# Kernel optimization log

Measured on AMD Instinct MI355X. Metric: run time of the kernel, lower is better.

## Reference

```python
import jax, jax.numpy as jnp
import numpy as np


def setup_inputs() -> dict:
    key = jax.random.key(0)
    ks = jax.random.split(key, 5)
    B, C, H, W = 4, 64, 64, 64
    C8 = C // 8
    return {
        "x_opt": jax.random.normal(ks[0], (B, C, H, W), jnp.float32),
        "x_sar": jax.random.normal(ks[1], (B, C, H, W), jnp.float32),
        "wq": jax.random.normal(ks[2], (C8, C), jnp.float32) * 0.05,
        "bq": jnp.zeros((C8,), jnp.float32),
        "wk": jax.random.normal(ks[3], (C8, C), jnp.float32) * 0.05,
        "bk": jnp.zeros((C8,), jnp.float32),
        "wv": jax.random.normal(ks[4], (C, C), jnp.float32) * 0.05,
        "bv": jnp.zeros((C,), jnp.float32),
        "gamma": jnp.zeros((1,), jnp.float32),
    }


def reference(x_opt, x_sar, wq, bq, wk, bk, wv, bv, gamma):
    b, c, h, w = x_opt.shape
    n = h * w
    xo = x_opt.reshape(b, c, n)  # [b, c, N]
    xs = x_sar.reshape(b, c, n)
    # 1x1 convs == channel matmuls
    q = jnp.einsum('oc,bcn->bon', wq, xo) + bq[None, :, None]  # [b, c//8, N]
    k = jnp.einsum('oc,bcn->bon', wk, xs) + bk[None, :, None]  # [b, c//8, N]
    v = jnp.einsum('oc,bcn->bon', wv, xs) + bv[None, :, None]  # [b, c, N]
    # attn[b, n, m] = softmax_m( q[:, :, n] . k[:, :, m] )  -- NO 1/sqrt(d) scaling
    scores = jnp.einsum('bdn,bdm->bnm', q, k)  # [b, N, N]
    attn = jax.nn.softmax(scores, axis=-1)
    # out[b, c, n] = sum_m v[b, c, m] * attn[b, n, m]
    out = jnp.einsum('bcm,bnm->bcn', v, attn).reshape(b, c, h, w)
    return gamma[0] * out + x_opt
```

## Files before the change

### kernel.cpp

```cpp
#include <hip/hip_runtime.h>
#include <hip/hip_bf16.h>
#include <stdint.h>

#define NDIM 4096
#define CDIM 64
#define NSPLIT 8
#define SPAN (NDIM / NSPLIT)
#define KBLK 128
#define NIT (SPAN / KBLK)
#define LOG2E 1.44269504088896f

typedef float f32x16 __attribute__((ext_vector_type(16)));
typedef short bf16x8 __attribute__((ext_vector_type(8)));
union U4B { uint4 u; bf16x8 b; };

static __device__ __forceinline__ uint32_t cvtpk(float lo, float hi) {
  uint32_t r;
  asm("v_cvt_pk_bf16_f32 %0, %1, %2" : "=v"(r) : "v"(lo), "v"(hi));
  return r;
}
static __device__ __forceinline__ uint16_t f2bf(float f) {
  uint32_t r;
  asm("v_cvt_pk_bf16_f32 %0, %1, %1" : "=v"(r) : "v"(f));
  return (uint16_t)r;
}
static __device__ __forceinline__ float fexp2(float x) {
  return __builtin_amdgcn_exp2f(x);
}
static __device__ __forceinline__ void gload_lds16(const void* g, void* l) {
  __builtin_amdgcn_global_load_lds(
      (const __attribute__((address_space(1))) uint32_t*)g,
      (__attribute__((address_space(3))) uint32_t*)l, 16, 0, 0);
}

__global__ __launch_bounds__(256) void proj_kernel(
    const float* __restrict__ x_opt, const float* __restrict__ x_sar,
    const float* __restrict__ wq, const float* __restrict__ bq,
    const float* __restrict__ wk, const float* __restrict__ bk,
    const float* __restrict__ wvp, const float* __restrict__ bv,
    uint16_t* __restrict__ qf, uint16_t* __restrict__ kf,
    uint16_t* __restrict__ vf)
{
  const int tid = threadIdx.x;
  const int w = tid >> 6;
  const int l = tid & 63;
  const int x = l & 31;
  const int hi = l >> 5;

  const int id = blockIdx.x;
  const int b = id >> 7;
  const int n0 = (id & 127) * 32;
  const size_t xbase = (size_t)b * CDIM * NDIM;

  const float* xsrc = (w == 2) ? x_opt : x_sar;
  bf16x8 xB[4];
#pragma unroll
  for (int kc = 0; kc < 4; kc++) {
    float sv[8];
#pragma unroll
    for (int j = 0; j < 8; j++)
      sv[j] = xsrc[xbase + (size_t)(kc * 16 + hi * 8 + j) * NDIM + n0 + x];
    U4B us;
    us.u = make_uint4(cvtpk(sv[0], sv[1]), cvtpk(sv[2], sv[3]),
                      cvtpk(sv[4], sv[5]), cvtpk(sv[6], sv[7]));
    xB[kc] = us.b;
  }

  bf16x8 aF[4];
#pragma unroll
  for (int kc = 0; kc < 4; kc++) {
    U4B ua;
    ua.u = make_uint4(0u, 0u, 0u, 0u);
    if (w < 2) {
      const float* wr = wvp + (w * 32 + x) * 64 + kc * 16 + hi * 8;
      float4 wa = ((const float4*)wr)[0];
      float4 wb = ((const float4*)wr)[1];
      ua.u = make_uint4(cvtpk(wa.x, wa.y), cvtpk(wa.z, wa.w),
                        cvtpk(wb.x, wb.y), cvtpk(wb.z, wb.w));
    } else if (x < 8) {
      const float* wr = ((w == 2) ? wq : wk) + x * 64 + kc * 16 + hi * 8;
      float4 wa = ((const float4*)wr)[0];
      float4 wb = ((const float4*)wr)[1];
      ua.u = make_uint4(cvtpk(wa.x, wa.y), cvtpk(wa.z, wa.w),
                        cvtpk(wb.x, wb.y), cvtpk(wb.z, wb.w));
    }
    aF[kc] = ua.b;
  }

  const f32x16 z16 = {0.f,0.f,0.f,0.f, 0.f,0.f,0.f,0.f,
                      0.f,0.f,0.f,0.f, 0.f,0.f,0.f,0.f};
  f32x16 acc = z16;
#pragma unroll
  for (int kc = 0; kc < 4; kc++)
    acc = __builtin_amdgcn_mfma_f32_32x32x16_bf16(aF[kc], xB[kc], acc, 0, 0, 0);

  if (w < 2) {
#pragma unroll
    for (int r = 0; r < 16; r++) {
      const int row = w * 32 + (r & 3) + 8 * (r >> 2) + 4 * hi;
      vf[(size_t)(b * 64 + row) * NDIM + n0 + x] = f2bf(acc[r] + bv[row]);
    }
  } else {
    const float* bias = (w == 2) ? bq : bk;
    const float scl = (w == 2) ? LOG2E : 1.0f;
    float gv[4];
#pragma unroll
    for (int r = 0; r < 4; r++) gv[r] = (acc[r] + bias[4 * hi + r]) * scl;
    uint16_t* dst = (w == 2) ? qf : kf;
    const size_t nrow = ((size_t)b * NDIM + n0 + x) * 16;
    uint2 st;
    st.x = cvtpk(gv[0], gv[1]); st.y = cvtpk(gv[2], gv[3]);
    *(uint2*)(dst + nrow + hi * 4) = st;
    if (hi == 0) {
      const uint4 z4 = make_uint4(0u, 0u, 0u, 0u);
      *(uint4*)(dst + nrow + 8) = z4;
    }
  }
}

__global__ __launch_bounds__(256, 4) void attn_kernel(
    const uint16_t* __restrict__ qf, const uint16_t* __restrict__ kf,
    const uint16_t* __restrict__ vf,
    uint16_t* __restrict__ po, float* __restrict__ ls)
{
  __shared__ __align__(16) uint16_t vt[2][64][128];

  const int tid = threadIdx.x;
  const int w = tid >> 6;
  const int l = tid & 63;
  const int x = l & 31;
  const int hi = l >> 5;

  const int id = blockIdx.x;
  const int sp = id & 7;
  const int qb = (id >> 3) & 31;
  const int b = id >> 8;

  const int n0 = qb * 128;
  const uint16_t* vsrc = vf + (size_t)b * CDIM * NDIM + sp * SPAN;
  const uint16_t* ksrc = kf + ((size_t)b * NDIM + sp * SPAN) * 16;
  const int qrow = n0 + w * 32 + x;

  U4B qfr;
  qfr.u = *(const uint4*)(qf + ((size_t)b * NDIM + qrow) * 16 + hi * 8);

  const uint32_t xh4 = (uint32_t)(((x & 15) ^ hi) << 4);
  const uint8_t* vbase0 = (const uint8_t*)&vt[0][0][0] + (size_t)x * 256;
  const uint8_t* vbase1 = vbase0 + 16384;

  const f32x16 z16 = {0.f,0.f,0.f,0.f, 0.f,0.f,0.f,0.f,
                      0.f,0.f,0.f,0.f, 0.f,0.f,0.f,0.f};
  f32x16 oacc0 = z16, oacc1 = z16;
  float lacc[4] = {0.f, 0.f, 0.f, 0.f};

  auto stageV = [&](int t, int buf) {
#pragma unroll
    for (int si = 0; si < 4; si++) {
      const int rowbase = w * 16 + si * 4;
      const int row = rowbase + (l >> 4);
      gload_lds16(vsrc + (size_t)row * NDIM + t * KBLK +
                      (((l & 15) ^ (row & 15)) << 3),
                  &vt[buf][rowbase][0]);
    }
  };

  stageV(0, 0);
  uint4 kc = *(const uint4*)(ksrc + (size_t)x * 16 + hi * 8);
  __syncthreads();

#pragma unroll
  for (int gq = 0; gq < 16; gq++) {
    const int it = gq >> 2;
    const int q4 = gq & 3;

    if (q4 == 0 && it + 1 < NIT) stageV(it + 1, (it + 1) & 1);

    uint4 kn = *(const uint4*)(ksrc + ((size_t)(gq + 1) * 32 + x) * 16 + hi * 8);

    U4B ka; ka.u = kc;
    f32x16 s = __builtin_amdgcn_mfma_f32_32x32x16_bf16(ka.b, qfr.b, z16, 0, 0, 0);

    float p[16];
#pragma unroll
    for (int i = 0; i < 16; i++) p[i] = fexp2(s[i]);
    float t8[8];
#pragma unroll
    for (int i = 0; i < 8; i++) t8[i] = p[i] + p[i + 8];
#pragma unroll
    for (int i = 0; i < 4; i++) lacc[i] += t8[i] + t8[i + 4];

    uint32_t W[8];
#pragma unroll
    for (int j = 0; j < 8; j++) W[j] = cvtpk(p[2 * j], p[2 * j + 1]);

    const uint8_t* vb = (it & 1) ? vbase1 : vbase0;
    __builtin_amdgcn_s_setprio(1);
#pragma unroll
    for (int sub = 0; sub < 2; sub++) {
      uint32_t a0 = W[sub * 4 + 0], b0 = W[sub * 4 + 2];
      uint32_t a1 = W[sub * 4 + 1], b1 = W[sub * 4 + 3];
      asm("v_permlane32_swap_b32 %0, %1" : "+v"(a0), "+v"(b0));
      asm("v_permlane32_swap_b32 %0, %1" : "+v"(a1), "+v"(b1));
      U4B pf;
      pf.u = make_uint4(a0, a1, b0, b1);
      const uint32_t kb4 = (uint32_t)((q4 * 4 + sub * 2) << 4);
      const uint8_t* va = vb + (kb4 ^ xh4);
      U4B vf0, vf1;
      vf0.u = *(const uint4*)(va);
      vf1.u = *(const uint4*)(va + 8192);
      oacc0 = __builtin_amdgcn_mfma_f32_32x32x16_bf16(vf0.b, pf.b, oacc0, 0, 0, 0);
      oacc1 = __builtin_amdgcn_mfma_f32_32x32x16_bf16(vf1.b, pf.b, oacc1, 0, 0, 0);
    }
    __builtin_amdgcn_s_setprio(0);

    if (q4 == 3) __syncthreads();
    kc = kn;
  }

  uint16_t* prow = po + (((size_t)sp * 4 + b) * NDIM + qrow) * CDIM;
#pragma unroll
  for (int cb = 0; cb < 2; cb++) {
    const f32x16 oa = (cb == 0) ? oacc0 : oacc1;
#pragma unroll
    for (int u = 0; u < 4; u++) {
      uint2 st;
      st.x = cvtpk(oa[u * 4 + 0], oa[u * 4 + 1]);
      st.y = cvtpk(oa[u * 4 + 2], oa[u * 4 + 3]);
      *(uint2*)(prow + cb * 32 + u * 8 + hi * 4) = st;
    }
  }
  float ltot = (lacc[0] + lacc[1]) + (lacc[2] + lacc[3]);
  ltot += __shfl_xor(ltot, 32);
  if (hi == 0)
    ls[((size_t)sp * 4 + b) * NDIM + qrow] = ltot;
}

__global__ __launch_bounds__(256) void merge_kernel(
    const uint16_t* __restrict__ po, const float* __restrict__ ls,
    const float* __restrict__ x_opt, const float* __restrict__ gamma,
    float* __restrict__ out)
{
  __shared__ float ot[32][65];
  const int tid = threadIdx.x;
  const int b = blockIdx.x >> 7;
  const int n0 = (blockIdx.x & 127) * 32;
  {
    const int q = tid >> 3;
    const int co = (tid & 7) * 8;
    const int nq = n0 + q;
    float wsum = 0.f;
    float acc[8] = {0.f, 0.f, 0.f, 0.f, 0.f, 0.f, 0.f, 0.f};
#pragma unroll
    for (int s = 0; s < NSPLIT; s++) {
      wsum += ls[((size_t)s * 4 + b) * NDIM + nq];
      const uint4 pv = *(const uint4*)(po + (((size_t)s * 4 + b) * NDIM + nq) * CDIM + co);
      const uint32_t* pw = (const uint32_t*)&pv;
#pragma unroll
      for (int j = 0; j < 4; j++) {
        acc[j * 2 + 0] += __uint_as_float(pw[j] << 16);
        acc[j * 2 + 1] += __uint_as_float(pw[j] & 0xFFFF0000u);
      }
    }
    const float inv = 1.f / wsum;
#pragma unroll
    for (int j = 0; j < 8; j++) ot[q][co + j] = acc[j] * inv;
  }
  __syncthreads();
  {
    const float gm = gamma[0];
    const int c = tid >> 2;
    const int j8 = (tid & 3) * 8;
    const float* xp = x_opt + ((size_t)b * CDIM + c) * NDIM + n0 + j8;
    float* op = out + ((size_t)b * CDIM + c) * NDIM + n0 + j8;
#pragma unroll
    for (int h = 0; h < 2; h++) {
      float4 xv = ((const float4*)xp)[h];
      float4 ov;
      ov.x = gm * ot[j8 + h * 4 + 0][c] + xv.x;
      ov.y = gm * ot[j8 + h * 4 + 1][c] + xv.y;
      ov.z = gm * ot[j8 + h * 4 + 2][c] + xv.z;
      ov.w = gm * ot[j8 + h * 4 + 3][c] + xv.w;
      ((float4*)op)[h] = ov;
    }
  }
}

extern "C" void kernel_launch(void* const* d_in, const int* in_sizes, int n_in,
                              void* d_out, int out_size, void* d_ws, size_t ws_size,
                              hipStream_t stream) {
  const float* x_opt = (const float*)d_in[0];
  const float* x_sar = (const float*)d_in[1];
  const float* wq    = (const float*)d_in[2];
  const float* bq    = (const float*)d_in[3];
  const float* wk    = (const float*)d_in[4];
  const float* bk    = (const float*)d_in[5];
  const float* wvp   = (const float*)d_in[6];
  const float* bv    = (const float*)d_in[7];
  const float* gamma = (const float*)d_in[8];
  float* outp = (float*)d_out;

  uint16_t* qf = (uint16_t*)d_ws;
  uint16_t* kf = (uint16_t*)((char*)d_ws + 524288);
  uint16_t* vf = (uint16_t*)((char*)d_ws + 1048576);
  uint16_t* po = (uint16_t*)((char*)d_ws + 3145728);
  float* lsp   = (float*)((char*)d_ws + 19922944);

  proj_kernel<<<512, 256, 0, stream>>>(x_opt, x_sar, wq, bq, wk, bk, wvp, bv,
                                       qf, kf, vf);
  attn_kernel<<<1024, 256, 0, stream>>>(qf, kf, vf, po, lsp);
  merge_kernel<<<512, 256, 0, stream>>>(po, lsp, x_opt, gamma, outp);
}
```

Baseline: 38.47 us.

## Load V fragments directly from global into registers, dropping LDS staging

The attention kernel no longer stages V tiles in shared memory through async global-to-LDS loads with a double buffer and barriers. Each lane now reads its V operand fragments straight from global memory into registers, prefetching one iteration ahead the same way K is prefetched. The exp/convert/row-sum loop is also fused so each probability is accumulated right after it is computed. This removes LDS traffic and the block-wide __syncthreads, but every wave now issues its own uncoalesced 16-byte global loads for V. Those loads are repeated across the waves of a block and raise register pressure under the 4-blocks-per-CU launch bound.

```diff
diff --git a/kernel.cpp b/kernel.cpp
--- a/kernel.cpp
+++ b/kernel.cpp
@@ -6,8 +6,6 @@
 #define CDIM 64
 #define NSPLIT 8
 #define SPAN (NDIM / NSPLIT)
-#define KBLK 128
-#define NIT (SPAN / KBLK)
 #define LOG2E 1.44269504088896f
 
 typedef float f32x16 __attribute__((ext_vector_type(16)));
@@ -26,11 +24,6 @@
 }
 static __device__ __forceinline__ float fexp2(float x) {
   return __builtin_amdgcn_exp2f(x);
-}
-static __device__ __forceinline__ void gload_lds16(const void* g, void* l) {
-  __builtin_amdgcn_global_load_lds(
-      (const __attribute__((address_space(1))) uint32_t*)g,
-      (__attribute__((address_space(3))) uint32_t*)l, 16, 0, 0);
 }
 
 __global__ __launch_bounds__(256) void proj_kernel(
@@ -123,8 +116,6 @@
     const uint16_t* __restrict__ vf,
     uint16_t* __restrict__ po, float* __restrict__ ls)
 {
-  __shared__ __align__(16) uint16_t vt[2][64][128];
-
   const int tid = threadIdx.x;
   const int w = tid >> 6;
   const int l = tid & 63;
@@ -137,84 +128,72 @@
   const int b = id >> 8;
 
   const int n0 = qb * 128;
-  const uint16_t* vsrc = vf + (size_t)b * CDIM * NDIM + sp * SPAN;
-  const uint16_t* ksrc = kf + ((size_t)b * NDIM + sp * SPAN) * 16;
   const int qrow = n0 + w * 32 + x;
 
   U4B qfr;
   qfr.u = *(const uint4*)(qf + ((size_t)b * NDIM + qrow) * 16 + hi * 8);
 
-  const uint32_t xh4 = (uint32_t)(((x & 15) ^ hi) << 4);
-  const uint8_t* vbase0 = (const uint8_t*)&vt[0][0][0] + (size_t)x * 256;
-  const uint8_t* vbase1 = vbase0 + 16384;
+  const uint16_t* kbase = kf + ((size_t)b * NDIM + sp * SPAN + x) * 16 + hi * 8;
+  const uint16_t* vbase0 = vf + ((size_t)(b * 64 + x)) * NDIM + sp * SPAN + hi * 8;
+  const uint16_t* vbase1 = vbase0 + (size_t)32 * NDIM;
 
   const f32x16 z16 = {0.f,0.f,0.f,0.f, 0.f,0.f,0.f,0.f,
                       0.f,0.f,0.f,0.f, 0.f,0.f,0.f,0.f};
   f32x16 oacc0 = z16, oacc1 = z16;
   float lacc[4] = {0.f, 0.f, 0.f, 0.f};
 
-  auto stageV = [&](int t, int buf) {
-#pragma unroll
-    for (int si = 0; si < 4; si++) {
-      const int rowbase = w * 16 + si * 4;
-      const int row = rowbase + (l >> 4);
-      gload_lds16(vsrc + (size_t)row * NDIM + t * KBLK +
-                      (((l & 15) ^ (row & 15)) << 3),
-                  &vt[buf][rowbase][0]);
-    }
-  };
-
-  stageV(0, 0);
-  uint4 kc = *(const uint4*)(ksrc + (size_t)x * 16 + hi * 8);
-  __syncthreads();
+  uint4 kc  = *(const uint4*)(kbase);
+  uint4 vc0 = *(const uint4*)(vbase0);
+  uint4 vc1 = *(const uint4*)(vbase0 + 16);
+  uint4 vd0 = *(const uint4*)(vbase1);
+  uint4 vd1 = *(const uint4*)(vbase1 + 16);
 
 #pragma unroll
   for (int gq = 0; gq < 16; gq++) {
-    const int it = gq >> 2;
-    const int q4 = gq & 3;
-
-    if (q4 == 0 && it + 1 < NIT) stageV(it + 1, (it + 1) & 1);
-
-    uint4 kn = *(const uint4*)(ksrc + ((size_t)(gq + 1) * 32 + x) * 16 + hi * 8);
+    const int ko = (gq + 1) * 512;
+    const int vo = (gq + 1) * 32;
+    uint4 kn  = *(const uint4*)(kbase + ko);
+    uint4 vn0 = *(const uint4*)(vbase0 + vo);
+    uint4 vn1 = *(const uint4*)(vbase0 + vo + 16);
+    uint4 vm0 = *(const uint4*)(vbase1 + vo);
+    uint4 vm1 = *(const uint4*)(vbase1 + vo + 16);
 
     U4B ka; ka.u = kc;
     f32x16 s = __builtin_amdgcn_mfma_f32_32x32x16_bf16(ka.b, qfr.b, z16, 0, 0, 0);
 
-    float p[16];
-#pragma unroll
-    for (int i = 0; i < 16; i++) p[i] = fexp2(s[i]);
-    float t8[8];
-#pragma unroll
-    for (int i = 0; i < 8; i++) t8[i] = p[i] + p[i + 8];
-#pragma unroll
-    for (int i = 0; i < 4; i++) lacc[i] += t8[i] + t8[i + 4];
-
     uint32_t W[8];
 #pragma unroll
-    for (int j = 0; j < 8; j++) W[j] = cvtpk(p[2 * j], p[2 * j + 1]);
-
-    const uint8_t* vb = (it & 1) ? vbase1 : vbase0;
+    for (int j = 0; j < 8; j++) {
+      const float p0 = fexp2(s[2 * j]);
+      const float p1 = fexp2(s[2 * j + 1]);
+      W[j] = cvtpk(p0, p1);
+      lacc[j & 3] += p0 + p1;
+    }
+
     __builtin_amdgcn_s_setprio(1);
-#pragma unroll
-    for (int sub = 0; sub < 2; sub++) {
-      uint32_t a0 = W[sub * 4 + 0], b0 = W[sub * 4 + 2];
-      uint32_t a1 = W[sub * 4 + 1], b1 = W[sub * 4 + 3];
+    {
+      uint32_t a0 = W[0], b0 = W[2], a1 = W[1], b1 = W[3];
       asm("v_permlane32_swap_b32 %0, %1" : "+v"(a0), "+v"(b0));
       asm("v_permlane32_swap_b32 %0, %1" : "+v"(a1), "+v"(b1));
-      U4B pf;
+      U4B pf, va, vb;
       pf.u = make_uint4(a0, a1, b0, b1);
-      const uint32_t kb4 = (uint32_t)((q4 * 4 + sub * 2) << 4);
-      const uint8_t* va = vb + (kb4 ^ xh4);
-      U4B vf0, vf1;
-      vf0.u = *(const uint4*)(va);
-      vf1.u = *(const uint4*)(va + 8192);
-      oacc0 = __builtin_amdgcn_mfma_f32_32x32x16_bf16(vf0.b, pf.b, oacc0, 0, 0, 0);
-      oacc1 = __builtin_amdgcn_mfma_f32_32x32x16_bf16(vf1.b, pf.b, oacc1, 0, 0, 0);
+      va.u = vc0; vb.u = vd0;
+      oacc0 = __builtin_amdgcn_mfma_f32_32x32x16_bf16(va.b, pf.b, oacc0, 0, 0, 0);
+      oacc1 = __builtin_amdgcn_mfma_f32_32x32x16_bf16(vb.b, pf.b, oacc1, 0, 0, 0);
+    }
+    {
+      uint32_t a0 = W[4], b0 = W[6], a1 = W[5], b1 = W[7];
+      asm("v_permlane32_swap_b32 %0, %1" : "+v"(a0), "+v"(b0));
+      asm("v_permlane32_swap_b32 %0, %1" : "+v"(a1), "+v"(b1));
+      U4B pf, va, vb;
+      pf.u = make_uint4(a0, a1, b0, b1);
+      va.u = vc1; vb.u = vd1;
+      oacc0 = __builtin_amdgcn_mfma_f32_32x32x16_bf16(va.b, pf.b, oacc0, 0, 0, 0);
+      oacc1 = __builtin_amdgcn_mfma_f32_32x32x16_bf16(vb.b, pf.b, oacc1, 0, 0, 0);
     }
     __builtin_amdgcn_s_setprio(0);
 
-    if (q4 == 3) __syncthreads();
-    kc = kn;
+    kc = kn; vc0 = vn0; vc1 = vn1; vd0 = vm0; vd1 = vm1;
   }
 
   uint16_t* prow = po + (((size_t)sp * 4 + b) * NDIM + qrow) * CDIM;
```

After: 55.46 us. +44.1%, slower.
